# Performance work log

Hardware: AMD Instinct MI355X
Metric: run time of the kernel (lower is better)

Reference implementation:

```python
import jax, jax.numpy as jnp
import numpy as np

N_CELL, N_DRUG = 8192, 4096


def setup_inputs() -> dict:
    key = jax.random.key(0)
    adj = jax.random.uniform(key, (N_CELL, N_DRUG), dtype=jnp.float32)
    return {"adj": adj}


def reference(adj):
    # Degree normalizations with +1 self-loop smoothing, as in the torch module.
    d_x = (jnp.sum(adj, axis=1) + 1.0) ** -0.5  # [N_CELL]
    d_y = (jnp.sum(adj, axis=0) + 1.0) ** -0.5  # [N_DRUG]

    # diag(d_x) @ adj @ diag(d_y) == row/col broadcast scaling (same math, O(n^2)).
    agg_cell_lp = d_x[:, None] * adj * d_y[None, :]          # [N_CELL, N_DRUG]
    agg_drug_lp = d_y[:, None] * adj.T * d_x[None, :]        # [N_DRUG, N_CELL]

    d_c = (jnp.sum(adj, axis=1) + 1.0) ** -1.0               # [N_CELL]
    self_cell_lp = jnp.diag(d_c + 1.0)                       # [N_CELL, N_CELL]
    d_d = (jnp.sum(adj, axis=0) + 1.0) ** -1.0               # [N_DRUG]
    self_drug_lp = jnp.diag(d_d + 1.0)                       # [N_DRUG, N_DRUG]

    return (agg_cell_lp, agg_drug_lp, self_cell_lp, self_drug_lp)
```

## Files before the change

kernel.cpp:

```cpp
#include <hip/hip_runtime.h>

#define N_CELL 8192
#define N_DRUG 4096

typedef float f32x4 __attribute__((ext_vector_type(4)));

static constexpr size_t OFF1 = (size_t)N_CELL * N_DRUG;
static constexpr size_t OFF2 = 2ull * N_CELL * N_DRUG;
static constexpr size_t OFF3 = OFF2 + (size_t)N_CELL * N_CELL;
static constexpr size_t FILL_F4 = ((size_t)N_CELL * N_CELL + (size_t)N_DRUG * N_DRUG) / 4;

#define FILL_BLOCKS 2048
static constexpr size_t FILL_PER_BLOCK = FILL_F4 / FILL_BLOCKS;

__global__ __launch_bounds__(256) void fill_kernel(float* __restrict__ fill_base) {
    f32x4 z = {0.f, 0.f, 0.f, 0.f};
    f32x4* p = reinterpret_cast<f32x4*>(fill_base) + (size_t)blockIdx.x * FILL_PER_BLOCK;
#pragma unroll 4
    for (size_t i = threadIdx.x; i < FILL_PER_BLOCK; i += 256) {
        __builtin_nontemporal_store(z, p + i);
    }
}

__global__ __launch_bounds__(256) void sums_kernel(const float* __restrict__ adj,
                                                   float* __restrict__ rowsum,
                                                   float* __restrict__ colsum) {
    __shared__ float part[64][65];
    int tid = threadIdx.x;
    int cb = blockIdx.x & 3;
    int rb = blockIdx.x >> 2;
    int c0 = cb * 1024;
    int r0 = rb * 64;
    const f32x4* ap = reinterpret_cast<const f32x4*>(adj + (size_t)r0 * N_DRUG + c0) + tid;
    f32x4 cacc = {0.f, 0.f, 0.f, 0.f};
#pragma unroll 4
    for (int r = 0; r < 64; ++r) {
        f32x4 v = ap[(size_t)r * (N_DRUG / 4)];
        cacc += v;
        float h = (v.x + v.y) + (v.z + v.w);
        h += __shfl_down(h, 1, 64);
        h += __shfl_down(h, 2, 64);
        if ((tid & 3) == 0) part[r][tid >> 2] = h;
    }
    __syncthreads();
    if (tid < 64) {
        float s = 0.f;
#pragma unroll 8
        for (int j = 0; j < 64; ++j) s += part[tid][j];
        atomicAdd(&rowsum[r0 + tid], s);
    }
    int c = c0 + tid * 4;
    atomicAdd(&colsum[c + 0], cacc.x);
    atomicAdd(&colsum[c + 1], cacc.y);
    atomicAdd(&colsum[c + 2], cacc.z);
    atomicAdd(&colsum[c + 3], cacc.w);
}

#define DIAG_BLOCKS 48
__global__ __launch_bounds__(256) void scale_kernel(const float* __restrict__ adj,
                                                    const float* __restrict__ rowsum,
                                                    const float* __restrict__ colsum,
                                                    float* __restrict__ out) {
    int tid = threadIdx.x;
    int b = blockIdx.x;
    if (b < DIAG_BLOCKS) {
        int idx = b * 256 + tid;
        if (idx < N_CELL) {
            out[OFF2 + (size_t)idx * (N_CELL + 1)] = 1.0f / (rowsum[idx] + 1.0f) + 1.0f;
        } else {
            int k = idx - N_CELL;
            out[OFF3 + (size_t)k * (N_DRUG + 1)] = 1.0f / (colsum[k] + 1.0f) + 1.0f;
        }
        return;
    }
    __shared__ float lds[64][69];
    int t = b - DIAG_BLOCKS;
    int tx = tid & 15;
    int ty = tid >> 4;
    int c0 = (t & 31) * 128;
    int r0 = (t >> 5) * 128;
    float* aggd = out + OFF1;
#pragma unroll
    for (int s = 0; s < 4; ++s) {
        int cc = c0 + (s & 1) * 64;
        int rr0 = r0 + (s >> 1) * 64;
        f32x4 cs = *reinterpret_cast<const f32x4*>(colsum + cc + tx * 4);
        f32x4 dy;
        dy.x = rsqrtf(cs.x + 1.0f);
        dy.y = rsqrtf(cs.y + 1.0f);
        dy.z = rsqrtf(cs.z + 1.0f);
        dy.w = rsqrtf(cs.w + 1.0f);
#pragma unroll
        for (int q = 0; q < 4; ++q) {
            int rr = q * 16 + ty;
            int r = rr0 + rr;
            float dx = rsqrtf(rowsum[r] + 1.0f);
            f32x4 v = *reinterpret_cast<const f32x4*>(adj + (size_t)r * N_DRUG + cc + tx * 4);
            f32x4 o = v * dx;
            o *= dy;
            __builtin_nontemporal_store(
                o, reinterpret_cast<f32x4*>(out + (size_t)r * N_DRUG + cc + tx * 4));
            lds[rr][tx * 4 + 0] = o.x;
            lds[rr][tx * 4 + 1] = o.y;
            lds[rr][tx * 4 + 2] = o.z;
            lds[rr][tx * 4 + 3] = o.w;
        }
        __syncthreads();
#pragma unroll
        for (int q = 0; q < 4; ++q) {
            int dr = q * 16 + ty;
            f32x4 o;
            o.x = lds[tx * 4 + 0][dr];
            o.y = lds[tx * 4 + 1][dr];
            o.z = lds[tx * 4 + 2][dr];
            o.w = lds[tx * 4 + 3][dr];
            __builtin_nontemporal_store(
                o, reinterpret_cast<f32x4*>(aggd + (size_t)(cc + dr) * N_CELL + rr0 + tx * 4));
        }
        __syncthreads();
    }
}

extern "C" void kernel_launch(void* const* d_in, const int* in_sizes, int n_in,
                              void* d_out, int out_size, void* d_ws, size_t ws_size,
                              hipStream_t stream) {
    const float* adj = (const float*)d_in[0];
    float* out = (float*)d_out;
    float* rowsum = (float*)d_ws;
    float* colsum = rowsum + N_CELL;

    (void)hipMemsetAsync(d_ws, 0, (N_CELL + N_DRUG) * sizeof(float), stream);

    fill_kernel<<<FILL_BLOCKS, 256, 0, stream>>>(out + OFF2);
    sums_kernel<<<512, 256, 0, stream>>>(adj, rowsum, colsum);
    scale_kernel<<<DIAG_BLOCKS + 2048, 256, 0, stream>>>(adj, rowsum, colsum, out);
}
```

Measured before the change: 174.3 us.

## Merge zero-fill and sums kernels into one launch; reorder diag blocks last

Combines the diagonal-matrix zero fill and the row/column sum reduction into a single kernel with block-index dispatch, so the bandwidth-bound fill overlaps with the adj read instead of running serially. Sum blocks come first so the reduction starts early. The fill now uses fewer, larger blocks. In the scale kernel the diagonal-writing blocks move to the end of the grid, occupancy hints are added to both kernels, and the inner tile loop is no longer unrolled. Fewer fill blocks and the no-unroll loop could cut memory-level parallelism.

```diff
diff --git a/kernel.cpp b/kernel.cpp
--- a/kernel.cpp
+++ b/kernel.cpp
@@ -10,27 +10,29 @@
 static constexpr size_t OFF3 = OFF2 + (size_t)N_CELL * N_CELL;
 static constexpr size_t FILL_F4 = ((size_t)N_CELL * N_CELL + (size_t)N_DRUG * N_DRUG) / 4;
 
-#define FILL_BLOCKS 2048
+#define SUM_BLOCKS 512
+#define FILL_BLOCKS 1280
+#define MEGA_BLOCKS (SUM_BLOCKS + FILL_BLOCKS)
 static constexpr size_t FILL_PER_BLOCK = FILL_F4 / FILL_BLOCKS;
 
-__global__ __launch_bounds__(256) void fill_kernel(float* __restrict__ fill_base) {
-    f32x4 z = {0.f, 0.f, 0.f, 0.f};
-    f32x4* p = reinterpret_cast<f32x4*>(fill_base) + (size_t)blockIdx.x * FILL_PER_BLOCK;
+__global__ __launch_bounds__(256, 8) void mega_kernel(const float* __restrict__ adj,
+                                                      float* __restrict__ rowsum,
+                                                      float* __restrict__ colsum,
+                                                      float* __restrict__ fill_base) {
+    int b = blockIdx.x;
+    int tid = threadIdx.x;
+    if (b >= SUM_BLOCKS) {
+        f32x4 z = {0.f, 0.f, 0.f, 0.f};
+        f32x4* p = reinterpret_cast<f32x4*>(fill_base) + (size_t)(b - SUM_BLOCKS) * FILL_PER_BLOCK;
 #pragma unroll 4
-    for (size_t i = threadIdx.x; i < FILL_PER_BLOCK; i += 256) {
-        __builtin_nontemporal_store(z, p + i);
+        for (size_t i = tid; i < FILL_PER_BLOCK; i += 256) {
+            __builtin_nontemporal_store(z, p + i);
+        }
+        return;
     }
-}
-
-__global__ __launch_bounds__(256) void sums_kernel(const float* __restrict__ adj,
-                                                   float* __restrict__ rowsum,
-                                                   float* __restrict__ colsum) {
     __shared__ float part[64][65];
-    int tid = threadIdx.x;
-    int cb = blockIdx.x & 3;
-    int rb = blockIdx.x >> 2;
-    int c0 = cb * 1024;
-    int r0 = rb * 64;
+    int cb = b & 3, rb = b >> 2;
+    int c0 = cb * 1024, r0 = rb * 64;
     const f32x4* ap = reinterpret_cast<const f32x4*>(adj + (size_t)r0 * N_DRUG + c0) + tid;
     f32x4 cacc = {0.f, 0.f, 0.f, 0.f};
 #pragma unroll 4
@@ -56,15 +58,16 @@
     atomicAdd(&colsum[c + 3], cacc.w);
 }
 
+#define SCALE_TILES 2048
 #define DIAG_BLOCKS 48
-__global__ __launch_bounds__(256) void scale_kernel(const float* __restrict__ adj,
-                                                    const float* __restrict__ rowsum,
-                                                    const float* __restrict__ colsum,
-                                                    float* __restrict__ out) {
+__global__ __launch_bounds__(256, 8) void scale_kernel(const float* __restrict__ adj,
+                                                       const float* __restrict__ rowsum,
+                                                       const float* __restrict__ colsum,
+                                                       float* __restrict__ out) {
     int tid = threadIdx.x;
     int b = blockIdx.x;
-    if (b < DIAG_BLOCKS) {
-        int idx = b * 256 + tid;
+    if (b >= SCALE_TILES) {
+        int idx = (b - SCALE_TILES) * 256 + tid;
         if (idx < N_CELL) {
             out[OFF2 + (size_t)idx * (N_CELL + 1)] = 1.0f / (rowsum[idx] + 1.0f) + 1.0f;
         } else {
@@ -74,13 +77,12 @@
         return;
     }
     __shared__ float lds[64][69];
-    int t = b - DIAG_BLOCKS;
     int tx = tid & 15;
     int ty = tid >> 4;
-    int c0 = (t & 31) * 128;
-    int r0 = (t >> 5) * 128;
+    int c0 = (b & 31) * 128;
+    int r0 = (b >> 5) * 128;
     float* aggd = out + OFF1;
-#pragma unroll
+#pragma unroll 1
     for (int s = 0; s < 4; ++s) {
         int cc = c0 + (s & 1) * 64;
         int rr0 = r0 + (s >> 1) * 64;
@@ -131,7 +133,6 @@
 
     (void)hipMemsetAsync(d_ws, 0, (N_CELL + N_DRUG) * sizeof(float), stream);
 
-    fill_kernel<<<FILL_BLOCKS, 256, 0, stream>>>(out + OFF2);
-    sums_kernel<<<512, 256, 0, stream>>>(adj, rowsum, colsum);
-    scale_kernel<<<DIAG_BLOCKS + 2048, 256, 0, stream>>>(adj, rowsum, colsum, out);
+    mega_kernel<<<MEGA_BLOCKS, 256, 0, stream>>>(adj, rowsum, colsum, out + OFF2);
+    scale_kernel<<<SCALE_TILES + DIAG_BLOCKS, 256, 0, stream>>>(adj, rowsum, colsum, out);
 }
```

New measurement: 152.7 us, median of 2. 12.4% less time.

## Fuse diagonal zero-fill into scale kernel and halve sum-kernel row tiles

Applied to the files above, without the earlier changes.

Removes the standalone zero-fill kernel and the dedicated diagonal blocks. Each scale tile now writes a slice of the two diagonal matrices after its transpose work, and computes the diagonal values in-line via modular index arithmetic. The sums kernel uses 32-row tiles with twice as many blocks for more parallelism, at the cost of more atomics. The fill loop adds an integer division per vector, and the scale loop is no longer unrolled.

```diff
diff --git a/kernel.cpp b/kernel.cpp
--- a/kernel.cpp
+++ b/kernel.cpp
@@ -1,4 +1,5 @@
 #include <hip/hip_runtime.h>
+#include <stdint.h>
 
 #define N_CELL 8192
 #define N_DRUG 4096
@@ -7,34 +8,23 @@
 
 static constexpr size_t OFF1 = (size_t)N_CELL * N_DRUG;
 static constexpr size_t OFF2 = 2ull * N_CELL * N_DRUG;
-static constexpr size_t OFF3 = OFF2 + (size_t)N_CELL * N_CELL;
-static constexpr size_t FILL_F4 = ((size_t)N_CELL * N_CELL + (size_t)N_DRUG * N_DRUG) / 4;
+static constexpr size_t CELLSZ = (size_t)N_CELL * N_CELL;
+static constexpr size_t FILL_F4 = (CELLSZ + (size_t)N_DRUG * N_DRUG) / 4;
 
-#define FILL_BLOCKS 2048
-static constexpr size_t FILL_PER_BLOCK = FILL_F4 / FILL_BLOCKS;
-
-__global__ __launch_bounds__(256) void fill_kernel(float* __restrict__ fill_base) {
-    f32x4 z = {0.f, 0.f, 0.f, 0.f};
-    f32x4* p = reinterpret_cast<f32x4*>(fill_base) + (size_t)blockIdx.x * FILL_PER_BLOCK;
-#pragma unroll 4
-    for (size_t i = threadIdx.x; i < FILL_PER_BLOCK; i += 256) {
-        __builtin_nontemporal_store(z, p + i);
-    }
-}
-
-__global__ __launch_bounds__(256) void sums_kernel(const float* __restrict__ adj,
-                                                   float* __restrict__ rowsum,
-                                                   float* __restrict__ colsum) {
-    __shared__ float part[64][65];
+#define SUM_BLOCKS 1024
+__global__ __launch_bounds__(256, 8) void sums_kernel(const float* __restrict__ adj,
+                                                      float* __restrict__ rowsum,
+                                                      float* __restrict__ colsum) {
+    __shared__ float part[32][65];
     int tid = threadIdx.x;
     int cb = blockIdx.x & 3;
     int rb = blockIdx.x >> 2;
     int c0 = cb * 1024;
-    int r0 = rb * 64;
+    int r0 = rb * 32;
     const f32x4* ap = reinterpret_cast<const f32x4*>(adj + (size_t)r0 * N_DRUG + c0) + tid;
     f32x4 cacc = {0.f, 0.f, 0.f, 0.f};
 #pragma unroll 4
-    for (int r = 0; r < 64; ++r) {
+    for (int r = 0; r < 32; ++r) {
         f32x4 v = ap[(size_t)r * (N_DRUG / 4)];
         cacc += v;
         float h = (v.x + v.y) + (v.z + v.w);
@@ -43,7 +33,7 @@
         if ((tid & 3) == 0) part[r][tid >> 2] = h;
     }
     __syncthreads();
-    if (tid < 64) {
+    if (tid < 32) {
         float s = 0.f;
 #pragma unroll 8
         for (int j = 0; j < 64; ++j) s += part[tid][j];
@@ -56,31 +46,22 @@
     atomicAdd(&colsum[c + 3], cacc.w);
 }
 
-#define DIAG_BLOCKS 48
-__global__ __launch_bounds__(256) void scale_kernel(const float* __restrict__ adj,
-                                                    const float* __restrict__ rowsum,
-                                                    const float* __restrict__ colsum,
-                                                    float* __restrict__ out) {
+#define SCALE_TILES 2048
+static constexpr uint32_t FILL_PER_BLOCK = (uint32_t)(FILL_F4 / SCALE_TILES);
+
+__global__ __launch_bounds__(256, 8) void scale_fill_kernel(const float* __restrict__ adj,
+                                                            const float* __restrict__ rowsum,
+                                                            const float* __restrict__ colsum,
+                                                            float* __restrict__ out) {
     int tid = threadIdx.x;
     int b = blockIdx.x;
-    if (b < DIAG_BLOCKS) {
-        int idx = b * 256 + tid;
-        if (idx < N_CELL) {
-            out[OFF2 + (size_t)idx * (N_CELL + 1)] = 1.0f / (rowsum[idx] + 1.0f) + 1.0f;
-        } else {
-            int k = idx - N_CELL;
-            out[OFF3 + (size_t)k * (N_DRUG + 1)] = 1.0f / (colsum[k] + 1.0f) + 1.0f;
-        }
-        return;
-    }
     __shared__ float lds[64][69];
-    int t = b - DIAG_BLOCKS;
     int tx = tid & 15;
     int ty = tid >> 4;
-    int c0 = (t & 31) * 128;
-    int r0 = (t >> 5) * 128;
+    int c0 = (b & 31) * 128;
+    int r0 = (b >> 5) * 128;
     float* aggd = out + OFF1;
-#pragma unroll
+#pragma unroll 1
     for (int s = 0; s < 4; ++s) {
         int cc = c0 + (s & 1) * 64;
         int rr0 = r0 + (s >> 1) * 64;
@@ -119,6 +100,33 @@
         }
         __syncthreads();
     }
+
+    f32x4* fp = reinterpret_cast<f32x4*>(out + OFF2);
+    const uint32_t CELL_F = (uint32_t)CELLSZ;
+    uint32_t base = (uint32_t)b * FILL_PER_BLOCK;
+#pragma unroll 4
+    for (uint32_t i = tid; i < FILL_PER_BLOCK; i += 256) {
+        uint32_t g = base + i;
+        uint32_t o = g * 4u;
+        f32x4 v = {0.f, 0.f, 0.f, 0.f};
+        if (o < CELL_F) {
+            uint32_t q = o / 8193u;
+            uint32_t m = o - q * 8193u;
+            if (m == 0u)         v.x = 1.0f / (rowsum[q] + 1.0f) + 1.0f;
+            else if (m == 8192u) v.y = 1.0f / (rowsum[q + 1] + 1.0f) + 1.0f;
+            else if (m == 8191u) v.z = 1.0f / (rowsum[q + 1] + 1.0f) + 1.0f;
+            else if (m == 8190u) v.w = 1.0f / (rowsum[q + 1] + 1.0f) + 1.0f;
+        } else {
+            uint32_t od = o - CELL_F;
+            uint32_t q = od / 4097u;
+            uint32_t m = od - q * 4097u;
+            if (m == 0u)         v.x = 1.0f / (colsum[q] + 1.0f) + 1.0f;
+            else if (m == 4096u) v.y = 1.0f / (colsum[q + 1] + 1.0f) + 1.0f;
+            else if (m == 4095u) v.z = 1.0f / (colsum[q + 1] + 1.0f) + 1.0f;
+            else if (m == 4094u) v.w = 1.0f / (colsum[q + 1] + 1.0f) + 1.0f;
+        }
+        __builtin_nontemporal_store(v, fp + g);
+    }
 }
 
 extern "C" void kernel_launch(void* const* d_in, const int* in_sizes, int n_in,
@@ -131,7 +139,6 @@
 
     (void)hipMemsetAsync(d_ws, 0, (N_CELL + N_DRUG) * sizeof(float), stream);
 
-    fill_kernel<<<FILL_BLOCKS, 256, 0, stream>>>(out + OFF2);
-    sums_kernel<<<512, 256, 0, stream>>>(adj, rowsum, colsum);
-    scale_kernel<<<DIAG_BLOCKS + 2048, 256, 0, stream>>>(adj, rowsum, colsum, out);
+    sums_kernel<<<SUM_BLOCKS, 256, 0, stream>>>(adj, rowsum, colsum);
+    scale_fill_kernel<<<SCALE_TILES, 256, 0, stream>>>(adj, rowsum, colsum, out);
 }
```

After: 177.9 us. 2.1% more time.
